# Kernel tuning notes

Hardware: AMD Instinct MI355X
Metric: run time of the kernel (lower is better)

The kernel has to match this reference:

```python
import jax, jax.numpy as jnp
import numpy as np

B, H, OUT, L_LAYERS = 64, 1024, 512, 2
SEQ = 256
SOS_VALUE = -2.0  # predict_binary_output=False


def setup_inputs() -> dict:
    key = jax.random.key(0)
    ks = jax.random.split(key, 16)
    s_ih0 = 1.0 / np.sqrt(OUT)
    s_h = 1.0 / np.sqrt(H)
    return {
        "encoder_output": jax.random.normal(ks[0], (B, SEQ, OUT), jnp.float32),
        "h0": jax.random.normal(ks[1], (L_LAYERS, B, H), jnp.float32),
        "c0": jax.random.normal(ks[2], (L_LAYERS, B, H), jnp.float32),
        "W_ih0": jax.random.normal(ks[3], (4 * H, OUT), jnp.float32) * s_ih0,
        "W_hh0": jax.random.normal(ks[4], (4 * H, H), jnp.float32) * s_h,
        "b_ih0": jax.random.normal(ks[5], (4 * H,), jnp.float32) * s_h,
        "b_hh0": jax.random.normal(ks[6], (4 * H,), jnp.float32) * s_h,
        "W_ih1": jax.random.normal(ks[7], (4 * H, H), jnp.float32) * s_h,
        "W_hh1": jax.random.normal(ks[8], (4 * H, H), jnp.float32) * s_h,
        "b_ih1": jax.random.normal(ks[9], (4 * H,), jnp.float32) * s_h,
        "b_hh1": jax.random.normal(ks[10], (4 * H,), jnp.float32) * s_h,
        "W_fc": jax.random.normal(ks[11], (OUT, H), jnp.float32) * s_h,
        "b_fc": jax.random.normal(ks[12], (OUT,), jnp.float32) * s_h,
        "seq_length": SEQ,
    }


def _lstm_cell(x, h, c, Wih, Whh, bih, bhh):
    # PyTorch gate order: i, f, g, o
    gates = x @ Wih.T + h @ Whh.T + (bih + bhh)
    i, f, g, o = jnp.split(gates, 4, axis=-1)
    i = jax.nn.sigmoid(i)
    f = jax.nn.sigmoid(f)
    g = jnp.tanh(g)
    o = jax.nn.sigmoid(o)
    c_new = f * c + i * g
    h_new = o * jnp.tanh(c_new)
    return h_new, c_new


def reference(encoder_output, h0, c0, W_ih0, W_hh0, b_ih0, b_hh0,
              W_ih1, W_hh1, b_ih1, b_hh1, W_fc, b_fc, seq_length):
    batch = h0.shape[1]
    y_init = jnp.full((batch, OUT), SOS_VALUE, dtype=h0.dtype)  # SOS token
    layers = ((W_ih0, W_hh0, b_ih0, b_hh0), (W_ih1, W_hh1, b_ih1, b_hh1))

    def step(carry, _):
        h, c, y = carry  # h, c: (num_layers, B, H); y: (B, OUT)
        x = y
        hs, cs = [], []
        for l, (Wih, Whh, bih, bhh) in enumerate(layers):
            h_l, c_l = _lstm_cell(x, h[l], c[l], Wih, Whh, bih, bhh)
            hs.append(h_l)
            cs.append(c_l)
            x = h_l
        y_hat = jax.nn.relu(x @ W_fc.T + b_fc)
        return (jnp.stack(hs), jnp.stack(cs), y_hat), y_hat

    (_, _, _), ys = jax.lax.scan(step, (h0, c0, y_init), None, length=seq_length)
    return jnp.transpose(ys, (1, 0, 2))  # (B, seq_length, OUT)
```

## Files before the change

### kernel.cpp

```cpp
#include <hip/hip_runtime.h>
#include <stdint.h>


#define NBLK 256
#define NTHR 256
#define HDIM 1024
#define ODIM 512
#define BDIM 64
#define SEQL 256

typedef _Float16 v8h __attribute__((ext_vector_type(8)));
typedef float    v4f __attribute__((ext_vector_type(4)));

#define WL0_NS 48
#define WL1_NS 64
#define WFC_NS 32
#define WL0_OFF 0
#define WL1_OFF (WL0_NS*1024)
#define WFC_OFF (WL1_OFF + WL1_NS*1024)
#define SMEM_BYTES (WFC_OFF + WFC_NS*1024)

#define YB_SZ  (BDIM*ODIM*2)
#define HB_SZ  (BDIM*HDIM*2)

#define FH0_REL 0
#define FH1_REL (4*256*4)
#define FY_REL  (FH1_REL + 4*256*4)
#define EH0_REL (FY_REL + 4*32*4)
#define EY_REL  (EH0_REL + 4*8*64)
#define FLG_BYTES (EY_REL + 4*8*64)

__device__ __forceinline__ float fsig(float x)   { return 1.0f / (1.0f + __expf(-x)); }
__device__ __forceinline__ float ftanhf(float x) { return 1.0f - 2.0f / (__expf(2.0f*x) + 1.0f); }

__device__ __forceinline__ unsigned long long ald8(const void* p){
  return __hip_atomic_load((const unsigned long long*)p, __ATOMIC_RELAXED, __HIP_MEMORY_SCOPE_AGENT);
}
__device__ __forceinline__ unsigned int ald4(const void* p){
  return __hip_atomic_load((const unsigned int*)p, __ATOMIC_RELAXED, __HIP_MEMORY_SCOPE_AGENT);
}
__device__ __forceinline__ void ast4(void* p, unsigned int v){
  __hip_atomic_store((unsigned int*)p, v, __ATOMIC_RELAXED, __HIP_MEMORY_SCOPE_AGENT);
}

__device__ __forceinline__ void wrap_inv(){
  asm volatile("s_waitcnt vmcnt(0)\n\tbuffer_inv sc1" ::: "memory");
}

__device__ __forceinline__ void wait_h_agg(const unsigned int* rowf, unsigned int* ep,
                                           int leader, unsigned int tag){
  if (leader){
    const char* p = (const char*)(rowf + (threadIdx.x & 63)*4);
    while (true){
      unsigned long long a = ald8(p);
      unsigned long long b = ald8(p+8);
      unsigned int m0 = (unsigned int)a, m1 = (unsigned int)(a >> 32);
      unsigned int m2 = (unsigned int)b, m3 = (unsigned int)(b >> 32);
      unsigned int m = min(min(m0, m1), min(m2, m3));
      if (__all(m >= tag)) break;
      __builtin_amdgcn_s_sleep(2);
    }
    if ((threadIdx.x & 63) == 0) ast4(ep, tag);
  } else {
    while (ald4(ep) < tag) __builtin_amdgcn_s_sleep(2);
  }
  asm volatile("" ::: "memory");
}

__device__ __forceinline__ void wait_y_agg(const unsigned int* rowf, unsigned int* ep,
                                           int leader, unsigned int tag){
  if (leader){
    const unsigned int* p = rowf + (threadIdx.x & 31);
    while (true){
      unsigned int v = ald4(p);
      if (__all(v >= tag)) break;
      __builtin_amdgcn_s_sleep(2);
    }
    if ((threadIdx.x & 63) == 0) ast4(ep, tag);
  } else {
    while (ald4(ep) < tag) __builtin_amdgcn_s_sleep(2);
  }
  asm volatile("" ::: "memory");
}

__device__ __forceinline__ void wait_grp256(const unsigned int* rowf, unsigned int tag){
  const char* p = (const char*)(rowf + (threadIdx.x & 63)*4);
  while (true){
    unsigned long long a = ald8(p);
    unsigned long long b = ald8(p+8);
    unsigned int m0 = (unsigned int)a, m1 = (unsigned int)(a >> 32);
    unsigned int m2 = (unsigned int)b, m3 = (unsigned int)(b >> 32);
    unsigned int m = min(min(m0, m1), min(m2, m3));
    if (__all(m >= tag)) break;
    __builtin_amdgcn_s_sleep(2);
  }
  asm volatile("" ::: "memory");
}

__device__ __forceinline__ void publish(unsigned int* flag, unsigned int tag){
  asm volatile("s_waitcnt vmcnt(0)" ::: "memory");
  if ((threadIdx.x & 63) == 0) ast4(flag, tag);
}

template<int NC>
__device__ __forceinline__ v4f gemm_phase(const char* const cb[], const char* wl, v4f acc){
  v8h A[4][8];
  constexpr int PF = (NC < 3) ? NC : 3;
  #pragma unroll
  for (int p = 0; p < PF; p++){
    #pragma unroll
    for (int j = 0; j < 8; j++) A[p][j] = *(const v8h*)(cb[p] + (size_t)j*64);
  }
  #pragma unroll
  for (int c = 0; c < NC; c++){
    const int cur = c & 3, nx = (c + 3) & 3;
    if (c + 3 < NC){
      #pragma unroll
      for (int j = 0; j < 8; j++) A[nx][j] = *(const v8h*)(cb[c+3] + (size_t)j*64);
    }
    #pragma unroll
    for (int j = 0; j < 8; j++){
      v8h B = *(const v8h*)(wl + (size_t)(c*8 + j)*1024);
      acc = __builtin_amdgcn_mfma_f32_16x16x32_f16(A[cur][j], B, acc, 0, 0, 0);
    }
  }
  return acc;
}

__device__ __forceinline__ void gemm_dual4(const char* const cb[], const char* wlA,
                                           const char* wlB, v4f& accA, v4f& accB){
  v8h A[4][8];
  #pragma unroll
  for (int p = 0; p < 3; p++){
    #pragma unroll
    for (int j = 0; j < 8; j++) A[p][j] = *(const v8h*)(cb[p] + (size_t)j*64);
  }
  #pragma unroll
  for (int c = 0; c < 4; c++){
    const int cur = c & 3, nx = (c + 3) & 3;
    if (c + 3 < 4){
      #pragma unroll
      for (int j = 0; j < 8; j++) A[nx][j] = *(const v8h*)(cb[c+3] + (size_t)j*64);
    }
    #pragma unroll
    for (int j = 0; j < 8; j++){
      v8h BA = *(const v8h*)(wlA + (size_t)(c*8 + j)*1024);
      accA = __builtin_amdgcn_mfma_f32_16x16x32_f16(A[cur][j], BA, accA, 0, 0, 0);
      v8h BB = *(const v8h*)(wlB + (size_t)(c*8 + j)*1024);
      accB = __builtin_amdgcn_mfma_f32_16x16x32_f16(A[cur][j], BB, accB, 0, 0, 0);
    }
  }
}

__device__ __forceinline__ void lstm_epi_pack(v4f acc, float bias, float* cs,
                                              char* hbase, int l15, int gidx){
  #pragma unroll
  for (int r = 0; r < 4; r++){
    float v  = acc[r] + bias;
    float x1 = __shfl_xor(v, 1);
    float x2 = __shfl_xor(v, 2);
    float x3 = __shfl_xor(v, 3);
    float vi = (gidx==0)?v :(gidx==1)?x1:(gidx==2)?x2:x3;
    float vf = (gidx==1)?v :(gidx==0)?x1:(gidx==3)?x2:x3;
    float vg = (gidx==2)?v :(gidx==3)?x1:(gidx==0)?x2:x3;
    float vo = (gidx==3)?v :(gidx==2)?x1:(gidx==1)?x2:x3;
    float ii = fsig(vi), ff = fsig(vf), gg = ftanhf(vg), oo = fsig(vo);
    float cn = ff*cs[r] + ii*gg;
    cs[r] = cn;
    float hn = oo * ftanhf(cn);
    unsigned int uv = (unsigned int)__builtin_bit_cast(unsigned short, (_Float16)hn);
    unsigned int o4 = (unsigned int)__shfl_xor((int)uv, 4);
    unsigned int pr = uv | (o4 << 16);
    unsigned int o8 = (unsigned int)__shfl_xor((int)pr, 8);
    if (l15 == 0){
      unsigned long long full = (unsigned long long)pr | ((unsigned long long)o8 << 32);
      __hip_atomic_store((unsigned long long*)(hbase + (size_t)r*(HDIM*2)), full,
                         __ATOMIC_RELAXED, __HIP_MEMORY_SCOPE_AGENT);
    }
  }
}

__global__ void init_kernel(const float* __restrict__ h0,
                            _Float16* __restrict__ h0bi, _Float16* __restrict__ h1bi,
                            _Float16* __restrict__ ybi){
  int i = blockIdx.x*256 + threadIdx.x;
  if (i < BDIM*HDIM){
    h0bi[i] = (_Float16)h0[i];
    h1bi[i] = (_Float16)h0[BDIM*HDIM + i];
  }
  if (i < BDIM*ODIM) ybi[i] = (_Float16)(-2.0f);
}

__launch_bounds__(NTHR, 1)
__global__ void decoder_kernel(
    const float* __restrict__ Wih0, const float* __restrict__ Whh0,
    const float* __restrict__ bih0, const float* __restrict__ bhh0,
    const float* __restrict__ Wih1, const float* __restrict__ Whh1,
    const float* __restrict__ bih1, const float* __restrict__ bhh1,
    const float* __restrict__ Wfc,  const float* __restrict__ bfc,
    const float* __restrict__ c0in, float* __restrict__ out,
    char* __restrict__ yB, char* __restrict__ h0B, char* __restrict__ h1B,
    char* __restrict__ flg, int dmask)
{
  extern __shared__ char smem[];
  const int bid = blockIdx.x;
  const int tid = threadIdx.x;
  const int wv  = tid >> 6;
  const int ln  = tid & 63;
  const int l15 = ln & 15;
  const int lq  = ln >> 4;
  const int u0  = bid * 4;
  const int xcd = bid & 7;
  const int leader = (bid < 8);

  unsigned int* fh0r = (unsigned int*)(flg + FH0_REL) + wv*256;
  unsigned int* fh1r = (unsigned int*)(flg + FH1_REL) + wv*256;
  unsigned int* fyr  = (unsigned int*)(flg + FY_REL)  + wv*32;
  unsigned int* eh0  = (unsigned int*)(flg + EH0_REL + (wv*8 + xcd)*64);
  unsigned int* ey   = (unsigned int*)(flg + EY_REL  + (wv*8 + xcd)*64);

  for (int slot = tid; slot < WL0_NS*64; slot += NTHR){
    int s = slot >> 6, l = slot & 63;
    int r16 = l & 15, q = l >> 4;
    int grow = (r16 & 3)*HDIM + u0 + (r16 >> 2);
    int kb = s*32 + q*8;
    const float* src; int k0;
    if (kb < ODIM){ src = Wih0 + (size_t)grow*ODIM; k0 = kb; }
    else          { src = Whh0 + (size_t)grow*HDIM; k0 = kb - ODIM; }
    v8h hv;
    #pragma unroll
    for (int j = 0; j < 8; j++) hv[j] = (_Float16)src[k0 + j];
    *(v8h*)(smem + WL0_OFF + s*1024 + l*16) = hv;
  }
  for (int slot = tid; slot < WL1_NS*64; slot += NTHR){
    int s = slot >> 6, l = slot & 63;
    int r16 = l & 15, q = l >> 4;
    int grow = (r16 & 3)*HDIM + u0 + (r16 >> 2);
    int kb = s*32 + q*8;
    const float* src; int k0;
    if (kb < HDIM){ src = Wih1 + (size_t)grow*HDIM; k0 = kb; }
    else          { src = Whh1 + (size_t)grow*HDIM; k0 = kb - HDIM; }
    v8h hv;
    #pragma unroll
    for (int j = 0; j < 8; j++) hv[j] = (_Float16)src[k0 + j];
    *(v8h*)(smem + WL1_OFF + s*1024 + l*16) = hv;
  }
  if (bid < 32){
    for (int slot = tid; slot < WFC_NS*64; slot += NTHR){
      int s = slot >> 6, l = slot & 63;
      int r16 = l & 15, q = l >> 4;
      const float* src = Wfc + (size_t)(bid*16 + r16)*HDIM;
      int k0 = s*32 + q*8;
      v8h hv;
      #pragma unroll
      for (int j = 0; j < 8; j++) hv[j] = (_Float16)src[k0 + j];
      *(v8h*)(smem + WFC_OFF + s*1024 + l*16) = hv;
    }
  }
  __syncthreads();

  const int gidx = l15 & 3;
  const int unit = u0 + (l15 >> 2);
  const int growL = gidx*HDIM + unit;
  const float bias0 = bih0[growL] + bhh0[growL];
  const float bias1 = bih1[growL] + bhh1[growL];
  float biasf = 0.f;
  if (bid < 32) biasf = bfc[bid*16 + l15];

  const int rb = wv*16 + lq*4;
  float cs0[4], cs1[4];
  #pragma unroll
  for (int r = 0; r < 4; r++){
    int b = rb + r;
    cs0[r] = c0in[(size_t)(0*BDIM + b)*HDIM + unit];
    cs1[r] = c0in[(size_t)(1*BDIM + b)*HDIM + unit];
  }

  const int row = wv*16 + l15;
  const size_t aoffY = (size_t)row*ODIM*2 + (size_t)lq*16;
  const size_t aoffH = (size_t)row*HDIM*2 + (size_t)lq*16;
  const size_t hwoff = ((size_t)rb*HDIM + u0)*2;
  const char* wl0 = smem + WL0_OFF + ln*16;
  const char* wl1 = smem + WL1_OFF + ln*16;
  const char* wlf = smem + WFC_OFF + ln*16;
  const char* wl0r = wl0 + 16*1024;
  const char* wl1r = wl1 + 32*1024;

  v4f p0 = {0.f,0.f,0.f,0.f};
  {
    const char* hi = h0B + (size_t)dmask*HB_SZ + aoffH;
    const char* cb[4] = { hi, hi+512, hi+1024, hi+1536 };
    p0 = gemm_phase<4>(cb, wl0r, p0);
  }

  for (int t = 0; t < SEQL; t++){
    const int sp = (t - 1) & dmask;
    const int sc = t & dmask;

    if ((t & dmask) == 0) wrap_inv();

    if (t > 0) wait_y_agg(fyr, ey, leader, (unsigned)t);

    {
      const char* ysrc = yB + (size_t)sp*YB_SZ + aoffY;
      const char* cb[2] = { ysrc, ysrc+512 };
      v4f acc = gemm_phase<2>(cb, wl0, p0);
      lstm_epi_pack(acc, bias0, cs0, h0B + (size_t)sc*HB_SZ + hwoff, l15, gidx);
    }
    publish(&fh0r[bid], (unsigned)(t+1));

    v4f p1 = {0.f,0.f,0.f,0.f};
    {
      const char* hs = h1B + (size_t)sp*HB_SZ + aoffH;
      const char* cb[4] = { hs, hs+512, hs+1024, hs+1536 };
      p1 = gemm_phase<4>(cb, wl1r, p1);
    }

    wait_h_agg(fh0r, eh0, leader, (unsigned)(t+1));

    {
      const char* hs = h0B + (size_t)sc*HB_SZ + aoffH;
      const char* cb[4] = { hs, hs+512, hs+1024, hs+1536 };
      v4f np0 = {0.f,0.f,0.f,0.f};
      gemm_dual4(cb, wl1, wl0r, p1, np0);
      lstm_epi_pack(p1, bias1, cs1, h1B + (size_t)sc*HB_SZ + hwoff, l15, gidx);
      p0 = np0;
    }
    publish(&fh1r[bid], (unsigned)(t+1));

    if (bid < 32){
      wait_grp256(fh1r, (unsigned)(t+1));
      const char* f = h1B + (size_t)sc*HB_SZ + aoffH;
      const char* cb[4] = { f, f+512, f+1024, f+1536 };
      v4f acc = {0.f,0.f,0.f,0.f};
      acc = gemm_phase<4>(cb, wlf, acc);
      char* ydst = yB + (size_t)sc*YB_SZ;
      #pragma unroll
      for (int r = 0; r < 4; r++){
        float v = fmaxf(acc[r] + biasf, 0.f);
        int b = rb + r;
        int o = bid*16 + l15;
        out[((size_t)b*SEQL + t)*ODIM + o] = v;
        unsigned int uv = (unsigned int)__builtin_bit_cast(unsigned short, (_Float16)v);
        unsigned int o1 = (unsigned int)__shfl_xor((int)uv, 1);
        unsigned int pr = uv | (o1 << 16);
        unsigned int o2 = (unsigned int)__shfl_xor((int)pr, 2);
        if ((l15 & 3) == 0){
          unsigned long long full = (unsigned long long)pr | ((unsigned long long)o2 << 32);
          __hip_atomic_store((unsigned long long*)(ydst + ((size_t)b*ODIM + o)*2),
                             full, __ATOMIC_RELAXED, __HIP_MEMORY_SCOPE_AGENT);
        }
      }
      publish(&fyr[bid], (unsigned)(t+1));
    }
  }
}

extern "C" void kernel_launch(void* const* d_in, const int* in_sizes, int n_in,
                              void* d_out, int out_size, void* d_ws, size_t ws_size,
                              hipStream_t stream){
  (void)in_sizes; (void)n_in; (void)out_size;

  int D = 16;
  while (D > 2 && (size_t)D*(YB_SZ + 2*HB_SZ) + FLG_BYTES > ws_size) D >>= 1;
  if ((size_t)D*(YB_SZ + 2*HB_SZ) + FLG_BYTES > ws_size) return;

  char* ws  = (char*)d_ws;
  char* yB  = ws;
  char* h0B = yB + (size_t)D*YB_SZ;
  char* h1B = h0B + (size_t)D*HB_SZ;
  char* flg = h1B + (size_t)D*HB_SZ;

  const float* h0   = (const float*)d_in[1];
  const float* c0   = (const float*)d_in[2];
  const float* Wih0 = (const float*)d_in[3];
  const float* Whh0 = (const float*)d_in[4];
  const float* bih0 = (const float*)d_in[5];
  const float* bhh0 = (const float*)d_in[6];
  const float* Wih1 = (const float*)d_in[7];
  const float* Whh1 = (const float*)d_in[8];
  const float* bih1 = (const float*)d_in[9];
  const float* bhh1 = (const float*)d_in[10];
  const float* Wfc  = (const float*)d_in[11];
  const float* bfc  = (const float*)d_in[12];
  float* out = (float*)d_out;

  (void)hipMemsetAsync(flg, 0, FLG_BYTES, stream);
  hipLaunchKernelGGL(init_kernel, dim3(256), dim3(256), 0, stream,
                     h0,
                     (_Float16*)(h0B + (size_t)(D-1)*HB_SZ),
                     (_Float16*)(h1B + (size_t)(D-1)*HB_SZ),
                     (_Float16*)(yB  + (size_t)(D-1)*YB_SZ));

  (void)hipFuncSetAttribute((const void*)decoder_kernel,
                            hipFuncAttributeMaxDynamicSharedMemorySize, SMEM_BYTES);
  hipLaunchKernelGGL(decoder_kernel, dim3(NBLK), dim3(NTHR), SMEM_BYTES, stream,
                     Wih0, Whh0, bih0, bhh0, Wih1, Whh1, bih1, bhh1,
                     Wfc, bfc, c0, out, yB, h0B, h1B, flg, D - 1);
}
```

Before: 5.431 ms.

## Split grid-wide flag waits into per-chunk waits overlapping GEMM chunks

Replaces the monolithic wait on all producer flags before each GEMM with per-quarter (h) and per-half (y) flag scans, so each K-chunk of the MFMA GEMM starts as soon as its slice of the input has been published. Leader blocks are moved from blocks 0-7 to 224-231 and publish per-chunk epoch words, followers spin on those words without sleep. The FC blocks likewise wait per quarter. The goal is to overlap synchronisation latency with compute, at the cost of more flag traffic, busy-spinning, and the loss of the old register prefetch pipeline across chunks.

```diff
diff --git a/kernel.cpp b/kernel.cpp
--- a/kernel.cpp
+++ b/kernel.cpp
@@ -8,6 +8,7 @@
 #define ODIM 512
 #define BDIM 64
 #define SEQL 256
+#define LEAD0 224
 
 typedef _Float16 v8h __attribute__((ext_vector_type(8)));
 typedef float    v4f __attribute__((ext_vector_type(4)));
@@ -33,9 +34,6 @@
 __device__ __forceinline__ float fsig(float x)   { return 1.0f / (1.0f + __expf(-x)); }
 __device__ __forceinline__ float ftanhf(float x) { return 1.0f - 2.0f / (__expf(2.0f*x) + 1.0f); }
 
-__device__ __forceinline__ unsigned long long ald8(const void* p){
-  return __hip_atomic_load((const unsigned long long*)p, __ATOMIC_RELAXED, __HIP_MEMORY_SCOPE_AGENT);
-}
 __device__ __forceinline__ unsigned int ald4(const void* p){
   return __hip_atomic_load((const unsigned int*)p, __ATOMIC_RELAXED, __HIP_MEMORY_SCOPE_AGENT);
 }
@@ -47,53 +45,24 @@
   asm volatile("s_waitcnt vmcnt(0)\n\tbuffer_inv sc1" ::: "memory");
 }
 
-__device__ __forceinline__ void wait_h_agg(const unsigned int* rowf, unsigned int* ep,
-                                           int leader, unsigned int tag){
-  if (leader){
-    const char* p = (const char*)(rowf + (threadIdx.x & 63)*4);
-    while (true){
-      unsigned long long a = ald8(p);
-      unsigned long long b = ald8(p+8);
-      unsigned int m0 = (unsigned int)a, m1 = (unsigned int)(a >> 32);
-      unsigned int m2 = (unsigned int)b, m3 = (unsigned int)(b >> 32);
-      unsigned int m = min(min(m0, m1), min(m2, m3));
-      if (__all(m >= tag)) break;
-      __builtin_amdgcn_s_sleep(2);
-    }
-    if ((threadIdx.x & 63) == 0) ast4(ep, tag);
-  } else {
-    while (ald4(ep) < tag) __builtin_amdgcn_s_sleep(2);
-  }
+__device__ __forceinline__ void wait_word(const unsigned int* w, unsigned int tag){
+  while (ald4(w) < tag) {}
   asm volatile("" ::: "memory");
 }
 
-__device__ __forceinline__ void wait_y_agg(const unsigned int* rowf, unsigned int* ep,
-                                           int leader, unsigned int tag){
-  if (leader){
-    const unsigned int* p = rowf + (threadIdx.x & 31);
-    while (true){
-      unsigned int v = ald4(p);
-      if (__all(v >= tag)) break;
-      __builtin_amdgcn_s_sleep(2);
-    }
-    if ((threadIdx.x & 63) == 0) ast4(ep, tag);
-  } else {
-    while (ald4(ep) < tag) __builtin_amdgcn_s_sleep(2);
-  }
+__device__ __forceinline__ void scan_quarter(const unsigned int* rowf, int q,
+                                             unsigned int* ew, unsigned int tag){
+  const unsigned int* p = rowf + q*64 + (threadIdx.x & 63);
+  while (!__all(ald4(p) >= tag)) __builtin_amdgcn_s_sleep(1);
+  if ((threadIdx.x & 63) == 0) ast4(ew + q, tag);
   asm volatile("" ::: "memory");
 }
 
-__device__ __forceinline__ void wait_grp256(const unsigned int* rowf, unsigned int tag){
-  const char* p = (const char*)(rowf + (threadIdx.x & 63)*4);
-  while (true){
-    unsigned long long a = ald8(p);
-    unsigned long long b = ald8(p+8);
-    unsigned int m0 = (unsigned int)a, m1 = (unsigned int)(a >> 32);
-    unsigned int m2 = (unsigned int)b, m3 = (unsigned int)(b >> 32);
-    unsigned int m = min(min(m0, m1), min(m2, m3));
-    if (__all(m >= tag)) break;
-    __builtin_amdgcn_s_sleep(2);
-  }
+__device__ __forceinline__ void scan_yhalf(const unsigned int* rowf, int h,
+                                           unsigned int* ew, unsigned int tag){
+  const unsigned int* p = rowf + h*16 + (threadIdx.x & 15);
+  while (!__all(ald4(p) >= tag)) __builtin_amdgcn_s_sleep(1);
+  if ((threadIdx.x & 63) == 0) ast4(ew + h, tag);
   asm volatile("" ::: "memory");
 }
 
@@ -102,54 +71,36 @@
   if ((threadIdx.x & 63) == 0) ast4(flag, tag);
 }
 
-template<int NC>
-__device__ __forceinline__ v4f gemm_phase(const char* const cb[], const char* wl, v4f acc){
-  v8h A[4][8];
-  constexpr int PF = (NC < 3) ? NC : 3;
-  #pragma unroll
-  for (int p = 0; p < PF; p++){
-    #pragma unroll
-    for (int j = 0; j < 8; j++) A[p][j] = *(const v8h*)(cb[p] + (size_t)j*64);
-  }
-  #pragma unroll
-  for (int c = 0; c < NC; c++){
-    const int cur = c & 3, nx = (c + 3) & 3;
-    if (c + 3 < NC){
-      #pragma unroll
-      for (int j = 0; j < 8; j++) A[nx][j] = *(const v8h*)(cb[c+3] + (size_t)j*64);
-    }
-    #pragma unroll
-    for (int j = 0; j < 8; j++){
-      v8h B = *(const v8h*)(wl + (size_t)(c*8 + j)*1024);
-      acc = __builtin_amdgcn_mfma_f32_16x16x32_f16(A[cur][j], B, acc, 0, 0, 0);
-    }
+__device__ __forceinline__ v4f chunk8(const char* abase, const char* wl, int c, v4f acc){
+  v8h A[8];
+  #pragma unroll
+  for (int j = 0; j < 8; j++) A[j] = *(const v8h*)(abase + (size_t)c*512 + (size_t)j*64);
+  #pragma unroll
+  for (int j = 0; j < 8; j++){
+    v8h B = *(const v8h*)(wl + (size_t)(c*8 + j)*1024);
+    acc = __builtin_amdgcn_mfma_f32_16x16x32_f16(A[j], B, acc, 0, 0, 0);
   }
   return acc;
 }
 
-__device__ __forceinline__ void gemm_dual4(const char* const cb[], const char* wlA,
-                                           const char* wlB, v4f& accA, v4f& accB){
-  v8h A[4][8];
-  #pragma unroll
-  for (int p = 0; p < 3; p++){
-    #pragma unroll
-    for (int j = 0; j < 8; j++) A[p][j] = *(const v8h*)(cb[p] + (size_t)j*64);
-  }
-  #pragma unroll
-  for (int c = 0; c < 4; c++){
-    const int cur = c & 3, nx = (c + 3) & 3;
-    if (c + 3 < 4){
-      #pragma unroll
-      for (int j = 0; j < 8; j++) A[nx][j] = *(const v8h*)(cb[c+3] + (size_t)j*64);
-    }
-    #pragma unroll
-    for (int j = 0; j < 8; j++){
-      v8h BA = *(const v8h*)(wlA + (size_t)(c*8 + j)*1024);
-      accA = __builtin_amdgcn_mfma_f32_16x16x32_f16(A[cur][j], BA, accA, 0, 0, 0);
-      v8h BB = *(const v8h*)(wlB + (size_t)(c*8 + j)*1024);
-      accB = __builtin_amdgcn_mfma_f32_16x16x32_f16(A[cur][j], BB, accB, 0, 0, 0);
-    }
-  }
+__device__ __forceinline__ void chunk8_dual(const char* abase, const char* wlA,
+                                            const char* wlB, int c, v4f& a1, v4f& a2){
+  v8h A[8];
+  #pragma unroll
+  for (int j = 0; j < 8; j++) A[j] = *(const v8h*)(abase + (size_t)c*512 + (size_t)j*64);
+  #pragma unroll
+  for (int j = 0; j < 8; j++){
+    v8h BA = *(const v8h*)(wlA + (size_t)(c*8 + j)*1024);
+    a1 = __builtin_amdgcn_mfma_f32_16x16x32_f16(A[j], BA, a1, 0, 0, 0);
+    v8h BB = *(const v8h*)(wlB + (size_t)(c*8 + j)*1024);
+    a2 = __builtin_amdgcn_mfma_f32_16x16x32_f16(A[j], BB, a2, 0, 0, 0);
+  }
+}
+
+__device__ __forceinline__ v4f gemm4(const char* abase, const char* wl, v4f acc){
+  #pragma unroll
+  for (int c = 0; c < 4; c++) acc = chunk8(abase, wl, c, acc);
+  return acc;
 }
 
 __device__ __forceinline__ void lstm_epi_pack(v4f acc, float bias, float* cs,
@@ -210,14 +161,14 @@
   const int l15 = ln & 15;
   const int lq  = ln >> 4;
   const int u0  = bid * 4;
-  const int xcd = bid & 7;
-  const int leader = (bid < 8);
+  const int f   = bid & 7;
+  const int leader = (bid >= LEAD0 && bid < LEAD0 + 8);
 
   unsigned int* fh0r = (unsigned int*)(flg + FH0_REL) + wv*256;
   unsigned int* fh1r = (unsigned int*)(flg + FH1_REL) + wv*256;
   unsigned int* fyr  = (unsigned int*)(flg + FY_REL)  + wv*32;
-  unsigned int* eh0  = (unsigned int*)(flg + EH0_REL + (wv*8 + xcd)*64);
-  unsigned int* ey   = (unsigned int*)(flg + EY_REL  + (wv*8 + xcd)*64);
+  unsigned int* eh0w = (unsigned int*)(flg + EH0_REL + (wv*8 + f)*64);
+  unsigned int* eyw  = (unsigned int*)(flg + EY_REL  + (wv*8 + f)*64);
 
   for (int slot = tid; slot < WL0_NS*64; slot += NTHR){
     int s = slot >> 6, l = slot & 63;
@@ -286,12 +237,7 @@
   const char* wl0r = wl0 + 16*1024;
   const char* wl1r = wl1 + 32*1024;
 
-  v4f p0 = {0.f,0.f,0.f,0.f};
-  {
-    const char* hi = h0B + (size_t)dmask*HB_SZ + aoffH;
-    const char* cb[4] = { hi, hi+512, hi+1024, hi+1536 };
-    p0 = gemm_phase<4>(cb, wl0r, p0);
-  }
+  v4f p0 = gemm4(h0B + (size_t)dmask*HB_SZ + aoffH, wl0r, v4f{0.f,0.f,0.f,0.f});
 
   for (int t = 0; t < SEQL; t++){
     const int sp = (t - 1) & dmask;
@@ -299,41 +245,54 @@
 
     if ((t & dmask) == 0) wrap_inv();
 
-    if (t > 0) wait_y_agg(fyr, ey, leader, (unsigned)t);
-
     {
-      const char* ysrc = yB + (size_t)sp*YB_SZ + aoffY;
-      const char* cb[2] = { ysrc, ysrc+512 };
-      v4f acc = gemm_phase<2>(cb, wl0, p0);
+      const char* ybase = yB + (size_t)sp*YB_SZ + aoffY;
+      v4f acc = p0;
+      #pragma unroll
+      for (int h = 0; h < 2; h++){
+        if (t > 0){
+          if (leader) scan_yhalf(fyr, h, eyw, (unsigned)t);
+          else        wait_word(eyw + h, (unsigned)t);
+        }
+        acc = chunk8(ybase, wl0, h, acc);
+      }
       lstm_epi_pack(acc, bias0, cs0, h0B + (size_t)sc*HB_SZ + hwoff, l15, gidx);
     }
     publish(&fh0r[bid], (unsigned)(t+1));
 
-    v4f p1 = {0.f,0.f,0.f,0.f};
     {
-      const char* hs = h1B + (size_t)sp*HB_SZ + aoffH;
-      const char* cb[4] = { hs, hs+512, hs+1024, hs+1536 };
-      p1 = gemm_phase<4>(cb, wl1r, p1);
-    }
-
-    wait_h_agg(fh0r, eh0, leader, (unsigned)(t+1));
-
-    {
-      const char* hs = h0B + (size_t)sc*HB_SZ + aoffH;
-      const char* cb[4] = { hs, hs+512, hs+1024, hs+1536 };
-      v4f np0 = {0.f,0.f,0.f,0.f};
-      gemm_dual4(cb, wl1, wl0r, p1, np0);
+      const char* h1p = h1B + (size_t)sp*HB_SZ + aoffH;
+      const char* h0c = h0B + (size_t)sc*HB_SZ + aoffH;
+      v4f p1, np0 = {0.f,0.f,0.f,0.f};
+      if (leader){
+        #pragma unroll
+        for (int q = 0; q < 4; q++) scan_quarter(fh0r, q, eh0w, (unsigned)(t+1));
+        p1 = gemm4(h1p, wl1r, v4f{0.f,0.f,0.f,0.f});
+        #pragma unroll
+        for (int q = 0; q < 4; q++) chunk8_dual(h0c, wl1, wl0r, q, p1, np0);
+      } else {
+        p1 = gemm4(h1p, wl1r, v4f{0.f,0.f,0.f,0.f});
+        #pragma unroll
+        for (int q = 0; q < 4; q++){
+          wait_word(eh0w + q, (unsigned)(t+1));
+          chunk8_dual(h0c, wl1, wl0r, q, p1, np0);
+        }
+      }
       lstm_epi_pack(p1, bias1, cs1, h1B + (size_t)sc*HB_SZ + hwoff, l15, gidx);
       p0 = np0;
     }
     publish(&fh1r[bid], (unsigned)(t+1));
 
     if (bid < 32){
-      wait_grp256(fh1r, (unsigned)(t+1));
-      const char* f = h1B + (size_t)sc*HB_SZ + aoffH;
-      const char* cb[4] = { f, f+512, f+1024, f+1536 };
+      const char* f1 = h1B + (size_t)sc*HB_SZ + aoffH;
       v4f acc = {0.f,0.f,0.f,0.f};
-      acc = gemm_phase<4>(cb, wlf, acc);
+      #pragma unroll
+      for (int q = 0; q < 4; q++){
+        const unsigned int* pp = fh1r + q*64 + ln;
+        while (!__all(ald4(pp) >= (unsigned)(t+1))) __builtin_amdgcn_s_sleep(1);
+        asm volatile("" ::: "memory");
+        acc = chunk8(f1, wlf, q, acc);
+      }
       char* ydst = yB + (size_t)sc*YB_SZ;
       #pragma unroll
       for (int r = 0; r < 4; r++){
```

New measurement: 5.897 ms. 8.6% more time.

## Move aggregator leaders off FC blocks and defer output stores past publish

Applied to the files above, without the earlier changes.

The eight leader blocks that aggregate per-step readiness flags move from block ids 0-7 to 224-231, so they no longer also run the FC stage (blocks 0-31). Leaders now scan the h0 flags before their layer-1 recurrent GEMM, while the other blocks do that GEMM first and then wait on the aggregated word. The intent is to shorten the signalling path on the critical chain. The FC blocks now publish the y flag before writing the fp32 output, which takes the global store off the critical path. Spin sleeps are also shortened, which raises polling traffic on the flags.

```diff
diff --git a/kernel.cpp b/kernel.cpp
--- a/kernel.cpp
+++ b/kernel.cpp
@@ -8,6 +8,7 @@
 #define ODIM 512
 #define BDIM 64
 #define SEQL 256
+#define LEAD0 224
 
 typedef _Float16 v8h __attribute__((ext_vector_type(8)));
 typedef float    v4f __attribute__((ext_vector_type(4)));
@@ -47,39 +48,32 @@
   asm volatile("s_waitcnt vmcnt(0)\n\tbuffer_inv sc1" ::: "memory");
 }
 
-__device__ __forceinline__ void wait_h_agg(const unsigned int* rowf, unsigned int* ep,
-                                           int leader, unsigned int tag){
-  if (leader){
-    const char* p = (const char*)(rowf + (threadIdx.x & 63)*4);
-    while (true){
-      unsigned long long a = ald8(p);
-      unsigned long long b = ald8(p+8);
-      unsigned int m0 = (unsigned int)a, m1 = (unsigned int)(a >> 32);
-      unsigned int m2 = (unsigned int)b, m3 = (unsigned int)(b >> 32);
-      unsigned int m = min(min(m0, m1), min(m2, m3));
-      if (__all(m >= tag)) break;
-      __builtin_amdgcn_s_sleep(2);
-    }
-    if ((threadIdx.x & 63) == 0) ast4(ep, tag);
-  } else {
-    while (ald4(ep) < tag) __builtin_amdgcn_s_sleep(2);
-  }
+__device__ __forceinline__ void wait_word(const unsigned int* w, unsigned int tag){
+  while (ald4(w) < tag) __builtin_amdgcn_s_sleep(1);
   asm volatile("" ::: "memory");
 }
 
-__device__ __forceinline__ void wait_y_agg(const unsigned int* rowf, unsigned int* ep,
-                                           int leader, unsigned int tag){
-  if (leader){
-    const unsigned int* p = rowf + (threadIdx.x & 31);
-    while (true){
-      unsigned int v = ald4(p);
-      if (__all(v >= tag)) break;
-      __builtin_amdgcn_s_sleep(2);
-    }
-    if ((threadIdx.x & 63) == 0) ast4(ep, tag);
-  } else {
-    while (ald4(ep) < tag) __builtin_amdgcn_s_sleep(2);
-  }
+__device__ __forceinline__ void scan256_pub(const unsigned int* rowf, unsigned int* ew,
+                                            unsigned int tag){
+  const char* p = (const char*)(rowf + (threadIdx.x & 63)*4);
+  while (true){
+    unsigned long long a = ald8(p);
+    unsigned long long b = ald8(p+8);
+    unsigned int m0 = (unsigned int)a, m1 = (unsigned int)(a >> 32);
+    unsigned int m2 = (unsigned int)b, m3 = (unsigned int)(b >> 32);
+    unsigned int m = min(min(m0, m1), min(m2, m3));
+    if (__all(m >= tag)) break;
+    __builtin_amdgcn_s_sleep(1);
+  }
+  if ((threadIdx.x & 63) == 0) ast4(ew, tag);
+  asm volatile("" ::: "memory");
+}
+
+__device__ __forceinline__ void scan32_pub(const unsigned int* rowf, unsigned int* ew,
+                                           unsigned int tag){
+  const unsigned int* p = rowf + (threadIdx.x & 31);
+  while (!__all(ald4(p) >= tag)) __builtin_amdgcn_s_sleep(1);
+  if ((threadIdx.x & 63) == 0) ast4(ew, tag);
   asm volatile("" ::: "memory");
 }
 
@@ -92,7 +86,7 @@
     unsigned int m2 = (unsigned int)b, m3 = (unsigned int)(b >> 32);
     unsigned int m = min(min(m0, m1), min(m2, m3));
     if (__all(m >= tag)) break;
-    __builtin_amdgcn_s_sleep(2);
+    __builtin_amdgcn_s_sleep(1);
   }
   asm volatile("" ::: "memory");
 }
@@ -210,14 +204,14 @@
   const int l15 = ln & 15;
   const int lq  = ln >> 4;
   const int u0  = bid * 4;
-  const int xcd = bid & 7;
-  const int leader = (bid < 8);
+  const int f   = bid & 7;
+  const int leader = (bid >= LEAD0 && bid < LEAD0 + 8);
 
   unsigned int* fh0r = (unsigned int*)(flg + FH0_REL) + wv*256;
   unsigned int* fh1r = (unsigned int*)(flg + FH1_REL) + wv*256;
   unsigned int* fyr  = (unsigned int*)(flg + FY_REL)  + wv*32;
-  unsigned int* eh0  = (unsigned int*)(flg + EH0_REL + (wv*8 + xcd)*64);
-  unsigned int* ey   = (unsigned int*)(flg + EY_REL  + (wv*8 + xcd)*64);
+  unsigned int* eh0  = (unsigned int*)(flg + EH0_REL + (wv*8 + f)*64);
+  unsigned int* ey   = (unsigned int*)(flg + EY_REL  + (wv*8 + f)*64);
 
   for (int slot = tid; slot < WL0_NS*64; slot += NTHR){
     int s = slot >> 6, l = slot & 63;
@@ -299,7 +293,10 @@
 
     if ((t & dmask) == 0) wrap_inv();
 
-    if (t > 0) wait_y_agg(fyr, ey, leader, (unsigned)t);
+    if (t > 0){
+      if (leader) scan32_pub(fyr, ey, (unsigned)t);
+      else        wait_word(ey, (unsigned)t);
+    }
 
     {
       const char* ysrc = yB + (size_t)sp*YB_SZ + aoffY;
@@ -313,10 +310,14 @@
     {
       const char* hs = h1B + (size_t)sp*HB_SZ + aoffH;
       const char* cb[4] = { hs, hs+512, hs+1024, hs+1536 };
-      p1 = gemm_phase<4>(cb, wl1r, p1);
-    }
-
-    wait_h_agg(fh0r, eh0, leader, (unsigned)(t+1));
+      if (leader){
+        scan256_pub(fh0r, eh0, (unsigned)(t+1));
+        p1 = gemm_phase<4>(cb, wl1r, p1);
+      } else {
+        p1 = gemm_phase<4>(cb, wl1r, p1);
+        wait_word(eh0, (unsigned)(t+1));
+      }
+    }
 
     {
       const char* hs = h0B + (size_t)sc*HB_SZ + aoffH;
@@ -330,28 +331,35 @@
 
     if (bid < 32){
       wait_grp256(fh1r, (unsigned)(t+1));
-      const char* f = h1B + (size_t)sc*HB_SZ + aoffH;
-      const char* cb[4] = { f, f+512, f+1024, f+1536 };
+      const char* f1 = h1B + (size_t)sc*HB_SZ + aoffH;
+      const char* cb[4] = { f1, f1+512, f1+1024, f1+1536 };
       v4f acc = {0.f,0.f,0.f,0.f};
       acc = gemm_phase<4>(cb, wlf, acc);
       char* ydst = yB + (size_t)sc*YB_SZ;
+      float yv[4];
       #pragma unroll
       for (int r = 0; r < 4; r++){
         float v = fmaxf(acc[r] + biasf, 0.f);
-        int b = rb + r;
-        int o = bid*16 + l15;
-        out[((size_t)b*SEQL + t)*ODIM + o] = v;
+        yv[r] = v;
         unsigned int uv = (unsigned int)__builtin_bit_cast(unsigned short, (_Float16)v);
         unsigned int o1 = (unsigned int)__shfl_xor((int)uv, 1);
         unsigned int pr = uv | (o1 << 16);
         unsigned int o2 = (unsigned int)__shfl_xor((int)pr, 2);
         if ((l15 & 3) == 0){
+          int b = rb + r;
+          int o = bid*16 + l15;
           unsigned long long full = (unsigned long long)pr | ((unsigned long long)o2 << 32);
           __hip_atomic_store((unsigned long long*)(ydst + ((size_t)b*ODIM + o)*2),
                              full, __ATOMIC_RELAXED, __HIP_MEMORY_SCOPE_AGENT);
         }
       }
       publish(&fyr[bid], (unsigned)(t+1));
+      #pragma unroll
+      for (int r = 0; r < 4; r++){
+        int b = rb + r;
+        int o = bid*16 + l15;
+        out[((size_t)b*SEQL + t)*ODIM + o] = yv[r];
+      }
     }
   }
 }
```

New measurement: 5.753 ms. +5.9%, slower.
